# Optimization experiments

Measured on AMD Instinct MI355X. Metric: run time of the kernel, lower is better.

## Reference

```python
import jax, jax.numpy as jnp
import numpy as np

BATCH, NUM, CONS = 16384, 512, 512


def setup_inputs() -> dict:
    key = jax.random.key(0)
    k1, k2, k3, k4 = jax.random.split(key, 4)
    preds = jax.random.uniform(k1, (BATCH, NUM), dtype=jnp.float32)
    # sparse, mutually-exclusive binary body masks (a literal is pos or neg, not both)
    r = jax.random.randint(k2, (CONS, NUM), 0, 12)
    pos_body = (r == 0).astype(jnp.float32)
    neg_body = (r == 1).astype(jnp.float32)
    head_atom = jax.random.randint(k3, (CONS,), 0, NUM).astype(jnp.int32)
    head_sign = jax.random.randint(k4, (CONS,), 0, 2).astype(jnp.bool_)
    return {"preds": preds, "pos_body": pos_body, "neg_body": neg_body,
            "head_atom": head_atom, "head_sign": head_sign}


def reference(preds, pos_body, neg_body, head_atom, head_sign):
    # apply_iterative with goal=None: Gauss-Seidel sweep over constraints.
    # For constraint c: body value per atom j is pos_body[c,j]*(1-p[:,j]) or
    # neg_body[c,j]*p[:,j]; candidate = 1 - max(0, max_j body value);
    # then head literal is raised (positive) or lowered (negative).
    def step(p, xs):
        pos_row, neg_row, atom, sign = xs
        # [batch, num] elementwise; masks are disjoint so per-atom max == concat-max
        vals = jnp.maximum(pos_row[None, :] * (1.0 - p), neg_row[None, :] * p)
        cand = 1.0 - jnp.maximum(jnp.max(vals, axis=1), 0.0)  # zeros column in torch cat
        prev = jnp.take(p, atom, axis=1)  # [batch]
        upd = jnp.where(sign,
                        jnp.maximum(prev, cand),
                        jnp.minimum(prev, 1.0 - cand))
        p = jax.lax.dynamic_update_slice(p, upd[:, None], (0, atom))
        return p, None

    out, _ = jax.lax.scan(step, preds, (pos_body, neg_body, head_atom, head_sign))
    return out
```

## Files before the change

kernel.cpp:

```cpp
#include <hip/hip_runtime.h>

#define BATCH 16384
#define NUM   512
#define CONS  512
#define ROWS  8
#define ZOFF  (NUM*16)
#define OOFF  (NUM*16 + 128)
#define LDSB  (NUM*16 + 256)
#define NPAD  (CONS + 4)
#define RSTR  84

typedef _Float16 h2 __attribute__((ext_vector_type(2)));
static __device__ __forceinline__ h2 u2h(unsigned u){ return __builtin_bit_cast(h2,u); }
static __device__ __forceinline__ unsigned h2u(h2 h){ return __builtin_bit_cast(unsigned,h); }
static __device__ __forceinline__ h2 hmax2(h2 a,h2 b){ return __builtin_elementwise_max(a,b); }
static __device__ __forceinline__ h2 hmin2(h2 a,h2 b){ return __builtin_elementwise_min(a,b); }
template<int C>
static __device__ __forceinline__ h2 dppmax(h2 x) {
  unsigned v = (unsigned)__builtin_amdgcn_mov_dpp((int)h2u(x), C, 0xF, 0xF, true);
  return hmax2(x, u2h(v));
}

__global__ __launch_bounds__(64) void prep_kernel(
    const float* __restrict__ pos, const float* __restrict__ neg,
    const int* __restrict__ head_atom, const int* __restrict__ head_sign,
    unsigned* __restrict__ ents) {
  int c = blockIdx.x, lane = threadIdx.x;
  unsigned* rec = ents + (size_t)c * RSTR;
  if (c >= CONS) {
    for (int t = lane; t < RSTR; t += 64) {
      unsigned v = 0;
      if (t < 32)      { unsigned d = ZOFF + (unsigned)(t & 7) * 16u; v = d | (d << 16); }
      else if (t < 64) { unsigned d = OOFF + (unsigned)(t & 7) * 16u; v = d | (d << 16); }
      else if (t == 64) v = 0x8000u << 16;
      else if (t < 73) v = ZOFF;
      else if (t < 81) v = OOFF;
      rec[t] = v;
    }
    return;
  }
  __shared__ unsigned short LN[96], LP[96];
  __shared__ unsigned short slotN[64], slotP[64];
  __shared__ unsigned char usedN[64], usedP[64];
  __shared__ unsigned short spill[16][8];
  __shared__ int spn[16];
  __shared__ unsigned short exN[8], exP[8];
  __shared__ int exn, exp_;
  slotN[lane] = (unsigned short)(ZOFF + (lane & 7) * 16);
  slotP[lane] = (unsigned short)(OOFF + (lane & 7) * 16);
  usedN[lane] = 0;    usedP[lane] = 0;
  if (lane < 8) { exN[lane] = ZOFF; exP[lane] = OOFF; }
  if (lane < 16) spn[lane] = 0;
  __syncthreads();

  int hp1 = (c >= 1) ? head_atom[c-1] : -1;
  int hp2 = (c >= 2) ? head_atom[c-2] : -1;
  int nN = 0, nP = 0;
  bool fN1=false, fP1=false, fN2=false, fP2=false;
  for (int k = 0; k < NUM/64; ++k) {
    int a = k*64 + lane;
    bool ln = neg[(size_t)c*NUM + a] != 0.f;
    bool lp = pos[(size_t)c*NUM + a] != 0.f;
    bool n1 = ln && (a == hp1), n2 = ln && (a == hp2);
    bool p1 = lp && (a == hp1), p2 = lp && (a == hp2);
    fN1 |= (__ballot(n1) != 0ull); fN2 |= (__ballot(n2) != 0ull);
    fP1 |= (__ballot(p1) != 0ull); fP2 |= (__ballot(p2) != 0ull);
    bool kn = ln && !n1 && !n2;
    bool kp = lp && !p1 && !p2;
    unsigned long long mn = __ballot(kn), mp = __ballot(kp);
    unsigned long long lt = (1ull << lane) - 1ull;
    int rn = nN + (int)__popcll(mn & lt);
    int rp = nP + (int)__popcll(mp & lt);
    if (kn && rn < 96) LN[rn] = (unsigned short)a;
    if (kp && rp < 96) LP[rp] = (unsigned short)a;
    nN += (int)__popcll(mn);
    nP += (int)__popcll(mp);
  }
  __syncthreads();
  if (lane < 16) {
    int r = lane & 7;
    bool isP = lane >= 8;
    const unsigned short* L = isP ? LP : LN;
    int n = isP ? nP : nN; if (n > 96) n = 96;
    unsigned short* slot = isP ? slotP : slotN;
    unsigned char* used = isP ? usedP : usedN;
    int rr = 0;
    for (int t = 0; t < n; ++t) {
      int a = L[t];
      if ((a & 7) == r) {
        if (rr < 8) { int s = rr*8 + r; slot[s] = (unsigned short)(a*16); used[s] = 1; }
        else if (rr < 16) spill[lane][rr-8] = (unsigned short)(a*16);
        ++rr;
      }
    }
    spn[lane] = rr > 8 ? (rr > 16 ? 8 : rr - 8) : 0;
  }
  __syncthreads();
  if (lane < 2) {
    bool isP = lane == 1;
    unsigned short* slot = isP ? slotP : slotN;
    unsigned char* used = isP ? usedP : usedN;
    unsigned short* exb = isP ? exP : exN;
    int base = isP ? 8 : 0;
    int e = 0, scan = 0;
    for (int r = 0; r < 8; ++r) {
      int ns = spn[base + r];
      for (int k = 0; k < ns; ++k) {
        unsigned short v = spill[base + r][k];
        while (scan < 64 && used[scan]) ++scan;
        if (scan < 64) { slot[scan] = v; used[scan] = 1; }
        else if (e < 8) exb[e++] = v;
      }
    }
    if (isP) exp_ = e; else exn = e;
  }
  __syncthreads();

  int hc = head_atom[c];
  unsigned fl = 0;
  if (head_sign[c]) fl |= 1u;
  if (fN1) fl |= 2u;  if (fP1) fl |= 4u;
  if (fN2) fl |= 8u;  if (fP2) fl |= 16u;
  if (hc == hp1) fl |= 32u; else if (hc == hp2) fl |= 64u;
  fl |= ((unsigned)exn << 7) | ((unsigned)exp_ << 11);
  unsigned ho = (unsigned)hc * 16u;
  for (int t = lane; t < RSTR; t += 64) {
    unsigned v;
    if (t < 32) {
      int jp = t >> 4, g = t & 15;
      v = (unsigned)slotN[32*jp + g] | ((unsigned)slotN[32*jp + 16 + g] << 16);
    } else if (t < 64) {
      int tp = t - 32, jp = tp >> 4, g = tp & 15;
      v = (unsigned)slotP[32*jp + g] | ((unsigned)slotP[32*jp + 16 + g] << 16);
    } else if (t == 64) v = ho | (fl << 16);
    else if (t < 73) v = exN[t - 65];
    else if (t < 81) v = exP[t - 73];
    else v = 0;
    rec[t] = v;
  }
}

struct ENT { unsigned w0, w1, w2, w3, mh; };
struct RDv { h2 n0,n1,n2,n3,p0,p1,p2,p3,pv; unsigned mh; };
struct ST  { h2 braw, prevraw; unsigned ho, flu; };

static __device__ __forceinline__ ENT ldent(const unsigned* ents, int c, int g) {
  const unsigned* rec = ents + (size_t)c * RSTR;
  ENT e;
  e.w0 = rec[g]; e.w1 = rec[16+g]; e.w2 = rec[32+g]; e.w3 = rec[48+g];
  e.mh = rec[64];
  return e;
}
static __device__ __forceinline__ void issue_reads(const ENT& E, const char* Pb,
                                                   unsigned pr4, RDv& R) {
  R.n0 = *(const h2*)(Pb + ((E.w0 & 0xFFFFu) + pr4));
  R.n1 = *(const h2*)(Pb + ((E.w0 >> 16)     + pr4));
  R.n2 = *(const h2*)(Pb + ((E.w1 & 0xFFFFu) + pr4));
  R.n3 = *(const h2*)(Pb + ((E.w1 >> 16)     + pr4));
  R.p0 = *(const h2*)(Pb + ((E.w2 & 0xFFFFu) + pr4));
  R.p1 = *(const h2*)(Pb + ((E.w2 >> 16)     + pr4));
  R.p2 = *(const h2*)(Pb + ((E.w3 & 0xFFFFu) + pr4));
  R.p3 = *(const h2*)(Pb + ((E.w3 >> 16)     + pr4));
  R.pv = *(const h2*)(Pb + ((E.mh & 0xFFFFu) + pr4));
  R.mh = E.mh;
}
static __device__ __forceinline__ void combine(const RDv& R, const unsigned* ents,
                                               int c, const char* Pb, unsigned pr4, ST& S) {
  h2 aN = hmax2(hmax2(R.n0, R.n1), hmax2(R.n2, R.n3));
  h2 aP = hmin2(hmin2(R.p0, R.p1), hmin2(R.p2, R.p3));
  unsigned flu = ((unsigned)__builtin_amdgcn_readfirstlane((int)R.mh)) >> 16;
  if (flu & 0x7F80u) {
    const unsigned* rec = ents + (size_t)c * RSTR;
    unsigned xn = (flu >> 7) & 15u, xp = (flu >> 11) & 15u;
    for (unsigned j = 0; j < xn; ++j) aN = hmax2(aN, *(const h2*)(Pb + (rec[65+j] + pr4)));
    for (unsigned j = 0; j < xp; ++j) aP = hmin2(aP, *(const h2*)(Pb + (rec[73+j] + pr4)));
  }
  const h2 one2 = {(_Float16)1.f, (_Float16)1.f};
  h2 bp = hmax2(aN, one2 - aP);
  bp = dppmax<0xB1>(bp);
  bp = dppmax<0x4E>(bp);
  bp = dppmax<0x141>(bp);
  {
    auto sw = __builtin_amdgcn_permlane32_swap((int)h2u(bp), (int)h2u(bp), false, false);
    bp = hmax2(u2h((unsigned)sw[0]), u2h((unsigned)sw[1]));
  }
  S.braw = bp; S.prevraw = R.pv; S.ho = R.mh & 0xFFFFu; S.flu = flu;
}
static __device__ __forceinline__ h2 finalize(const ST& S, h2 up1, h2 up2,
                                              char* Pb, unsigned pr4, int lane) {
  const h2 one2 = {(_Float16)1.f, (_Float16)1.f};
  unsigned fl = S.flu;
  h2 b = S.braw;
  if (fl & 0x1Eu) {
    unsigned mN1 = 0u-((fl>>1)&1u), mP1 = 0u-((fl>>2)&1u);
    unsigned mN2 = 0u-((fl>>3)&1u), mP2 = 0u-((fl>>4)&1u);
    b = hmax2(b, u2h(h2u(up1) & mN1));
    b = hmax2(b, u2h(h2u(one2 - up1) & mP1));
    b = hmax2(b, u2h(h2u(up2) & mN2));
    b = hmax2(b, u2h(h2u(one2 - up2) & mP2));
  }
  h2 prev = S.prevraw;
  if (fl & 0x60u) {
    unsigned mR1 = 0u-((fl>>5)&1u), mR2 = 0u-((fl>>6)&1u), mRn = ~(mR1|mR2);
    prev = u2h((h2u(up1)&mR1) | (h2u(up2)&mR2) | (h2u(S.prevraw)&mRn));
  }
  unsigned ms = 0u-(fl&1u);
  unsigned hi = h2u(hmax2(prev, one2 - b));
  unsigned lo = h2u(hmin2(prev, b));
  h2 upd = u2h((hi&ms) | (lo&~ms));
  if ((lane & 39) == 0 && !(fl & 0x8000u))
    *(h2*)(Pb + S.ho + pr4) = upd;
  return upd;
}

__global__ __launch_bounds__(64, 2) void solve_kernel(
    const float* __restrict__ preds,
    const unsigned* __restrict__ ents,
    float* __restrict__ out) {
  __shared__ char Pb[LDSB];
  const int lane = threadIdx.x;
  const unsigned pr4 = (unsigned)((lane >> 3) & 3) * 4u;
  const int g = (lane & 7) | ((lane >> 5) << 3);
  const int r2s = lane >> 4, cs = lane & 15;
  const size_t row0 = (size_t)blockIdx.x * ROWS;

  if (lane < 32) *(unsigned*)(Pb + ZOFF + lane*4) = 0u;
  else           *(unsigned*)(Pb + OOFF + (lane-32)*4) = 0x3C003C00u;

  for (int i = 0; i < 16; ++i) {
    int a = i*32 + cs*2;
    float2 v0 = *(const float2*)(preds + (row0 + 2*r2s)     * NUM + a);
    float2 v1 = *(const float2*)(preds + (row0 + 2*r2s + 1) * NUM + a);
    h2 w0 = {(_Float16)v0.x, (_Float16)v1.x};
    h2 w1 = {(_Float16)v0.y, (_Float16)v1.y};
    *(h2*)(Pb + a*16 + r2s*4) = w0;
    *(h2*)(Pb + (a+1)*16 + r2s*4) = w1;
  }
  __syncthreads();

  ENT E0 = ldent(ents, 0, g), E1 = ldent(ents, 1, g);
  ENT E2 = ldent(ents, 2, g), E3 = ldent(ents, 3, g);
  RDv RA, RB; ST S0, S1;
  issue_reads(E0, Pb, pr4, RA);
  issue_reads(E1, Pb, pr4, RB);
  combine(RA, ents, 0, Pb, pr4, S0);
  h2 up1 = (h2)0.0f, up2 = (h2)0.0f;

  #pragma unroll 1
  for (int i = 0; i < CONS; i += 2) {
    issue_reads(E2, Pb, pr4, RA);
    { h2 u = finalize(S0, up1, up2, Pb, pr4, lane); up2 = up1; up1 = u; }
    combine(RB, ents, i+1, Pb, pr4, S1);
    E2 = ldent(ents, i+4, g);
    issue_reads(E3, Pb, pr4, RB);
    { h2 u = finalize(S1, up1, up2, Pb, pr4, lane); up2 = up1; up1 = u; }
    combine(RA, ents, i+2, Pb, pr4, S0);
    E3 = ldent(ents, i+5, g);
  }

  __syncthreads();
  for (int i = 0; i < 16; ++i) {
    int a = i*32 + cs*2;
    h2 w0 = *(const h2*)(Pb + a*16 + r2s*4);
    h2 w1 = *(const h2*)(Pb + (a+1)*16 + r2s*4);
    float2 v0 = {(float)w0.x, (float)w1.x};
    float2 v1 = {(float)w0.y, (float)w1.y};
    *(float2*)(out + (row0 + 2*r2s)     * NUM + a) = v0;
    *(float2*)(out + (row0 + 2*r2s + 1) * NUM + a) = v1;
  }
}

extern "C" void kernel_launch(void* const* d_in, const int* in_sizes, int n_in,
                              void* d_out, int out_size, void* d_ws, size_t ws_size,
                              hipStream_t stream) {
  (void)in_sizes; (void)n_in; (void)out_size; (void)ws_size;
  const float* preds     = (const float*)d_in[0];
  const float* pos       = (const float*)d_in[1];
  const float* neg       = (const float*)d_in[2];
  const int*   head_atom = (const int*)d_in[3];
  const int*   head_sign = (const int*)d_in[4];

  unsigned* ents = (unsigned*)d_ws;

  prep_kernel<<<NPAD, 64, 0, stream>>>(pos, neg, head_atom, head_sign, ents);
  solve_kernel<<<BATCH / ROWS, 64, 0, stream>>>(preds, ents, (float*)d_out);
}
```

Measured before the change: 273.7 us.

## Process two constraints per step across wavefront halves with four rows per block

Each workgroup now handles 4 batch rows instead of 8, and the two 32-lane halves of the wavefront evaluate consecutive constraints (a pair) at the same time. The second constraint's dependence on the first is resolved via permlane32 swap and flag masks. The prep kernel now builds paired records with 16 classes of 4 slots, spill handling, and a third-previous-head dependency flag. Occupancy rises to 4 waves per SIMD, and the serial chain per constraint pair gets shorter. The cost is extra select and mask logic, plus more complex and fragile encoding of the cases where the paired constraints depend on each other.

```diff
diff --git a/kernel.cpp b/kernel.cpp
--- a/kernel.cpp
+++ b/kernel.cpp
@@ -3,12 +3,13 @@
 #define BATCH 16384
 #define NUM   512
 #define CONS  512
-#define ROWS  8
-#define ZOFF  (NUM*16)
-#define OOFF  (NUM*16 + 128)
-#define LDSB  (NUM*16 + 256)
-#define NPAD  (CONS + 4)
-#define RSTR  84
+#define ROWS  4
+#define ZOFF  (NUM*8)
+#define OOFF  (NUM*8 + 128)
+#define LDSB  (NUM*8 + 256)
+#define NPAIR 260
+#define NPAD  (2*NPAIR)
+#define RSTR  148
 
 typedef _Float16 h2 __attribute__((ext_vector_type(2)));
 static __device__ __forceinline__ h2 u2h(unsigned u){ return __builtin_bit_cast(h2,u); }
@@ -20,6 +21,13 @@
   unsigned v = (unsigned)__builtin_amdgcn_mov_dpp((int)h2u(x), C, 0xF, 0xF, true);
   return hmax2(x, u2h(v));
 }
+static __device__ __forceinline__ h2 bmask(unsigned mh, int bit) {
+  return u2h((unsigned)(((int)(mh << (31 - bit))) >> 31));
+}
+static __device__ __forceinline__ h2 swap32pair(h2 x, bool hi) {
+  auto r = __builtin_amdgcn_permlane32_swap((int)h2u(x), (int)h2u(x), false, false);
+  return u2h((unsigned)(hi ? r[0] : r[1]));
+}
 
 __global__ __launch_bounds__(64) void prep_kernel(
     const float* __restrict__ pos, const float* __restrict__ neg,
@@ -27,246 +35,272 @@
     unsigned* __restrict__ ents) {
   int c = blockIdx.x, lane = threadIdx.x;
   unsigned* rec = ents + (size_t)c * RSTR;
-  if (c >= CONS) {
-    for (int t = lane; t < RSTR; t += 64) {
-      unsigned v = 0;
-      if (t < 32)      { unsigned d = ZOFF + (unsigned)(t & 7) * 16u; v = d | (d << 16); }
-      else if (t < 64) { unsigned d = OOFF + (unsigned)(t & 7) * 16u; v = d | (d << 16); }
-      else if (t == 64) v = 0x8000u << 16;
-      else if (t < 73) v = ZOFF;
-      else if (t < 81) v = OOFF;
-      rec[t] = v;
-    }
-    return;
-  }
-  __shared__ unsigned short LN[96], LP[96];
   __shared__ unsigned short slotN[64], slotP[64];
-  __shared__ unsigned char usedN[64], usedP[64];
-  __shared__ unsigned short spill[16][8];
-  __shared__ int spn[16];
+  __shared__ unsigned char  usedN[64], usedP[64];
+  __shared__ unsigned short spillN[16][12], spillP[16][12];
+  __shared__ unsigned char  spnN[16], spnP[16];
   __shared__ unsigned short exN[8], exP[8];
   __shared__ int exn, exp_;
-  slotN[lane] = (unsigned short)(ZOFF + (lane & 7) * 16);
-  slotP[lane] = (unsigned short)(OOFF + (lane & 7) * 16);
-  usedN[lane] = 0;    usedP[lane] = 0;
-  if (lane < 8) { exN[lane] = ZOFF; exP[lane] = OOFF; }
-  if (lane < 16) spn[lane] = 0;
+  slotN[lane] = (unsigned short)(ZOFF + (lane & 15) * 8);
+  slotP[lane] = (unsigned short)(OOFF + (lane & 15) * 8);
+  usedN[lane] = 0; usedP[lane] = 0;
+  if (lane < 8)  { exN[lane] = ZOFF; exP[lane] = OOFF; }
+  if (lane < 16) { spnN[lane] = 0;  spnP[lane] = 0; }
+  if (lane == 0) { exn = 0; exp_ = 0; }
   __syncthreads();
 
-  int hp1 = (c >= 1) ? head_atom[c-1] : -1;
-  int hp2 = (c >= 2) ? head_atom[c-2] : -1;
-  int nN = 0, nP = 0;
-  bool fN1=false, fP1=false, fN2=false, fP2=false;
-  for (int k = 0; k < NUM/64; ++k) {
-    int a = k*64 + lane;
-    bool ln = neg[(size_t)c*NUM + a] != 0.f;
-    bool lp = pos[(size_t)c*NUM + a] != 0.f;
-    bool n1 = ln && (a == hp1), n2 = ln && (a == hp2);
-    bool p1 = lp && (a == hp1), p2 = lp && (a == hp2);
-    fN1 |= (__ballot(n1) != 0ull); fN2 |= (__ballot(n2) != 0ull);
-    fP1 |= (__ballot(p1) != 0ull); fP2 |= (__ballot(p2) != 0ull);
-    bool kn = ln && !n1 && !n2;
-    bool kp = lp && !p1 && !p2;
-    unsigned long long mn = __ballot(kn), mp = __ballot(kp);
-    unsigned long long lt = (1ull << lane) - 1ull;
-    int rn = nN + (int)__popcll(mn & lt);
-    int rp = nP + (int)__popcll(mp & lt);
-    if (kn && rn < 96) LN[rn] = (unsigned short)a;
-    if (kp && rp < 96) LP[rp] = (unsigned short)a;
-    nN += (int)__popcll(mn);
-    nP += (int)__popcll(mp);
-  }
-  __syncthreads();
-  if (lane < 16) {
-    int r = lane & 7;
-    bool isP = lane >= 8;
-    const unsigned short* L = isP ? LP : LN;
-    int n = isP ? nP : nN; if (n > 96) n = 96;
-    unsigned short* slot = isP ? slotP : slotN;
-    unsigned char* used = isP ? usedP : usedN;
-    int rr = 0;
-    for (int t = 0; t < n; ++t) {
-      int a = L[t];
-      if ((a & 7) == r) {
-        if (rr < 8) { int s = rr*8 + r; slot[s] = (unsigned short)(a*16); used[s] = 1; }
-        else if (rr < 16) spill[lane][rr-8] = (unsigned short)(a*16);
-        ++rr;
+  unsigned fl = 0, ho = ZOFF;
+  if (c < CONS) {
+    int hp1 = (c >= 1) ? head_atom[c-1] : -1;
+    int hp2 = (c >= 2) ? head_atom[c-2] : -1;
+    int hp3 = ((c & 1) && c >= 3) ? head_atom[c-3] : -1;
+    bool fN1=false,fP1=false,fN2=false,fP2=false,fN3=false,fP3=false;
+    const int myclass = lane & 15;
+    const unsigned long long clsmask = 0x0001000100010001ull << myclass;
+    const unsigned long long lt = (1ull << lane) - 1ull;
+    int cntN = 0, cntP = 0;
+    for (int k = 0; k < NUM/64; ++k) {
+      int a = k*64 + lane;
+      bool ln = neg[(size_t)c*NUM + a] != 0.f;
+      bool lp = pos[(size_t)c*NUM + a] != 0.f;
+      bool i1 = (a == hp1);
+      bool i2 = (a == hp2) && !i1;
+      bool i3 = (a == hp3) && !i1 && (a != hp2);
+      fN1 |= __ballot(ln && i1) != 0ull; fP1 |= __ballot(lp && i1) != 0ull;
+      fN2 |= __ballot(ln && i2) != 0ull; fP2 |= __ballot(lp && i2) != 0ull;
+      fN3 |= __ballot(ln && i3) != 0ull; fP3 |= __ballot(lp && i3) != 0ull;
+      bool kn = ln && !i1 && !i2 && !i3;
+      bool kp = lp && !i1 && !i2 && !i3;
+      unsigned long long mn = __ballot(kn) & clsmask;
+      unsigned long long mp = __ballot(kp) & clsmask;
+      if (kn) {
+        int rr = cntN + (int)__popcll(mn & lt);
+        if (rr < 4) { slotN[rr*16+myclass] = (unsigned short)(a*8); usedN[rr*16+myclass] = 1; }
+        else if (rr < 16) spillN[myclass][rr-4] = (unsigned short)(a*8);
       }
+      if (kp) {
+        int rr = cntP + (int)__popcll(mp & lt);
+        if (rr < 4) { slotP[rr*16+myclass] = (unsigned short)(a*8); usedP[rr*16+myclass] = 1; }
+        else if (rr < 16) spillP[myclass][rr-4] = (unsigned short)(a*8);
+      }
+      cntN += (int)__popcll(mn); cntP += (int)__popcll(mp);
     }
-    spn[lane] = rr > 8 ? (rr > 16 ? 8 : rr - 8) : 0;
-  }
-  __syncthreads();
-  if (lane < 2) {
-    bool isP = lane == 1;
-    unsigned short* slot = isP ? slotP : slotN;
-    unsigned char* used = isP ? usedP : usedN;
-    unsigned short* exb = isP ? exP : exN;
-    int base = isP ? 8 : 0;
-    int e = 0, scan = 0;
-    for (int r = 0; r < 8; ++r) {
-      int ns = spn[base + r];
-      for (int k = 0; k < ns; ++k) {
-        unsigned short v = spill[base + r][k];
-        while (scan < 64 && used[scan]) ++scan;
-        if (scan < 64) { slot[scan] = v; used[scan] = 1; }
-        else if (e < 8) exb[e++] = v;
+    if (lane < 16) {
+      int sn = cntN - 4; if (sn < 0) sn = 0; if (sn > 12) sn = 12;
+      int sp = cntP - 4; if (sp < 0) sp = 0; if (sp > 12) sp = 12;
+      spnN[lane] = (unsigned char)sn; spnP[lane] = (unsigned char)sp;
+    }
+    __syncthreads();
+    if (lane < 2) {
+      bool isP = lane == 1;
+      unsigned short* slot = isP ? slotP : slotN;
+      unsigned char*  used = isP ? usedP : usedN;
+      unsigned char*  spn  = isP ? spnP  : spnN;
+      unsigned short* exb  = isP ? exP   : exN;
+      int e = 0, scan = 0;
+      for (int r = 0; r < 16; ++r) {
+        int ns = spn[r];
+        for (int k = 0; k < ns; ++k) {
+          unsigned short v = isP ? spillP[r][k] : spillN[r][k];
+          while (scan < 64 && used[scan]) ++scan;
+          if (scan < 64) { slot[scan] = v; used[scan] = 1; }
+          else if (e < 7) exb[e++] = v;
+        }
       }
+      if (isP) exp_ = e; else exn = e;
     }
-    if (isP) exp_ = e; else exn = e;
-  }
-  __syncthreads();
-
-  int hc = head_atom[c];
-  unsigned fl = 0;
-  if (head_sign[c]) fl |= 1u;
-  if (fN1) fl |= 2u;  if (fP1) fl |= 4u;
-  if (fN2) fl |= 8u;  if (fP2) fl |= 16u;
-  if (hc == hp1) fl |= 32u; else if (hc == hp2) fl |= 64u;
-  fl |= ((unsigned)exn << 7) | ((unsigned)exp_ << 11);
-  unsigned ho = (unsigned)hc * 16u;
+    __syncthreads();
+    int hc = head_atom[c];
+    fl = (head_sign[c] ? 1u : 0u)
+       | (fN1?2u:0u) | (fP1?4u:0u) | (fN2?8u:0u) | (fP2?16u:0u);
+    unsigned rcode = (hc==hp1) ? 1u : (hc==hp2) ? 2u : (hc==hp3) ? 3u : 0u;
+    fl |= rcode << 5;
+    fl |= ((unsigned)exn) << 7;
+    fl |= ((unsigned)exp_) << 10;
+    if (fN3) fl |= 1u << 13;
+    if (fP3) fl |= 1u << 14;
+    if (!(c & 1) && (c + 1) < CONS && head_atom[c+1] == hc) fl |= 0x8000u;
+    ho = (unsigned)hc * 8u;
+  } else {
+    fl = 0x8000u;
+  }
+
   for (int t = lane; t < RSTR; t += 64) {
     unsigned v;
-    if (t < 32) {
-      int jp = t >> 4, g = t & 15;
-      v = (unsigned)slotN[32*jp + g] | ((unsigned)slotN[32*jp + 16 + g] << 16);
-    } else if (t < 64) {
-      int tp = t - 32, jp = tp >> 4, g = tp & 15;
-      v = (unsigned)slotP[32*jp + g] | ((unsigned)slotP[32*jp + 16 + g] << 16);
-    } else if (t == 64) v = ho | (fl << 16);
-    else if (t < 73) v = exN[t - 65];
-    else if (t < 81) v = exP[t - 73];
+    if (t < 130) {
+      int copy = (t >= 65) ? 1 : 0;
+      int u = t - copy*65;
+      unsigned pr = (unsigned)copy * 4u;
+      if (u == 64) v = (ho + pr) | (fl << 16);
+      else {
+        int gg = u & 15, blk = u >> 4;
+        const unsigned short* arr = (blk >= 2) ? slotP : slotN;
+        int base = (blk & 1) * 32;
+        v = ((unsigned)arr[base+gg] + pr) | ((((unsigned)arr[base+16+gg]) + pr) << 16);
+      }
+    } else if (t < 138) v = exN[t-130];
+    else if (t < 146) v = exP[t-138];
     else v = 0;
     rec[t] = v;
   }
 }
 
-struct ENT { unsigned w0, w1, w2, w3, mh; };
-struct RDv { h2 n0,n1,n2,n3,p0,p1,p2,p3,pv; unsigned mh; };
-struct ST  { h2 braw, prevraw; unsigned ho, flu; };
-
-static __device__ __forceinline__ ENT ldent(const unsigned* ents, int c, int g) {
-  const unsigned* rec = ents + (size_t)c * RSTR;
-  ENT e;
-  e.w0 = rec[g]; e.w1 = rec[16+g]; e.w2 = rec[32+g]; e.w3 = rec[48+g];
-  e.mh = rec[64];
+struct PENT { unsigned r0, r1, r2, r3, rm; };
+struct RDv  { h2 n0,n1,n2,n3,p0,p1,p2,p3,pv; unsigned mh; };
+struct ST   { h2 bp, pv; unsigned mh, su; };
+
+static __device__ __forceinline__ PENT pld(const unsigned* ents, int p, int lo, int lm) {
+  const unsigned* bp = ents + (size_t)(2*p) * RSTR;
+  PENT e;
+  e.r0 = bp[lo]; e.r1 = bp[lo+16]; e.r2 = bp[lo+32]; e.r3 = bp[lo+48]; e.rm = bp[lm];
   return e;
 }
-static __device__ __forceinline__ void issue_reads(const ENT& E, const char* Pb,
-                                                   unsigned pr4, RDv& R) {
-  R.n0 = *(const h2*)(Pb + ((E.w0 & 0xFFFFu) + pr4));
-  R.n1 = *(const h2*)(Pb + ((E.w0 >> 16)     + pr4));
-  R.n2 = *(const h2*)(Pb + ((E.w1 & 0xFFFFu) + pr4));
-  R.n3 = *(const h2*)(Pb + ((E.w1 >> 16)     + pr4));
-  R.p0 = *(const h2*)(Pb + ((E.w2 & 0xFFFFu) + pr4));
-  R.p1 = *(const h2*)(Pb + ((E.w2 >> 16)     + pr4));
-  R.p2 = *(const h2*)(Pb + ((E.w3 & 0xFFFFu) + pr4));
-  R.p3 = *(const h2*)(Pb + ((E.w3 >> 16)     + pr4));
-  R.pv = *(const h2*)(Pb + ((E.mh & 0xFFFFu) + pr4));
-  R.mh = E.mh;
-}
-static __device__ __forceinline__ void combine(const RDv& R, const unsigned* ents,
-                                               int c, const char* Pb, unsigned pr4, ST& S) {
-  h2 aN = hmax2(hmax2(R.n0, R.n1), hmax2(R.n2, R.n3));
-  h2 aP = hmin2(hmin2(R.p0, R.p1), hmin2(R.p2, R.p3));
-  unsigned flu = ((unsigned)__builtin_amdgcn_readfirstlane((int)R.mh)) >> 16;
-  if (flu & 0x7F80u) {
-    const unsigned* rec = ents + (size_t)c * RSTR;
-    unsigned xn = (flu >> 7) & 15u, xp = (flu >> 11) & 15u;
-    for (unsigned j = 0; j < xn; ++j) aN = hmax2(aN, *(const h2*)(Pb + (rec[65+j] + pr4)));
-    for (unsigned j = 0; j < xp; ++j) aP = hmin2(aP, *(const h2*)(Pb + (rec[73+j] + pr4)));
+static __device__ __forceinline__ void issue(const PENT& E, const char* Pb, RDv& R) {
+  R.n0 = *(const h2*)(Pb + (E.r0 & 0xFFFFu));
+  R.n1 = *(const h2*)(Pb + (E.r0 >> 16));
+  R.n2 = *(const h2*)(Pb + (E.r1 & 0xFFFFu));
+  R.n3 = *(const h2*)(Pb + (E.r1 >> 16));
+  R.p0 = *(const h2*)(Pb + (E.r2 & 0xFFFFu));
+  R.p1 = *(const h2*)(Pb + (E.r2 >> 16));
+  R.p2 = *(const h2*)(Pb + (E.r3 & 0xFFFFu));
+  R.p3 = *(const h2*)(Pb + (E.r3 >> 16));
+  R.pv = *(const h2*)(Pb + (E.rm & 0xFFFFu));
+  R.mh = E.rm;
+}
+static __device__ __forceinline__ void comb(const RDv& R, const unsigned* __restrict__ ents,
+    int p, int half, unsigned pr4b, const char* Pb, ST& S) {
+  h2 aN = hmax2(hmax2(R.n0,R.n1), hmax2(R.n2,R.n3));
+  h2 aP = hmin2(hmin2(R.p0,R.p1), hmin2(R.p2,R.p3));
+  unsigned s0 = (unsigned)__builtin_amdgcn_readfirstlane((int)R.mh);
+  unsigned s1 = (unsigned)__builtin_amdgcn_readlane((int)R.mh, 32);
+  unsigned su = s0 | s1;
+  if (su & 0x1F800000u) {
+    unsigned xa = (s0>>23)&7u, xb = (s1>>23)&7u; unsigned xn = xa>xb?xa:xb;
+    unsigned ya = (s0>>26)&7u, yb = (s1>>26)&7u; unsigned xp = ya>yb?ya:yb;
+    const unsigned* rp_ = ents + (size_t)(2*p + half) * RSTR;
+    for (unsigned j = 0; j < xn; ++j) aN = hmax2(aN, *(const h2*)(Pb + (rp_[130+j] + pr4b)));
+    for (unsigned j = 0; j < xp; ++j) aP = hmin2(aP, *(const h2*)(Pb + (rp_[138+j] + pr4b)));
   }
   const h2 one2 = {(_Float16)1.f, (_Float16)1.f};
-  h2 bp = hmax2(aN, one2 - aP);
-  bp = dppmax<0xB1>(bp);
-  bp = dppmax<0x4E>(bp);
-  bp = dppmax<0x141>(bp);
-  {
-    auto sw = __builtin_amdgcn_permlane32_swap((int)h2u(bp), (int)h2u(bp), false, false);
-    bp = hmax2(u2h((unsigned)sw[0]), u2h((unsigned)sw[1]));
-  }
-  S.braw = bp; S.prevraw = R.pv; S.ho = R.mh & 0xFFFFu; S.flu = flu;
-}
-static __device__ __forceinline__ h2 finalize(const ST& S, h2 up1, h2 up2,
-                                              char* Pb, unsigned pr4, int lane) {
+  h2 b = hmax2(aN, one2 - aP);
+  b = dppmax<0xB1>(b);
+  b = dppmax<0x4E>(b);
+  b = dppmax<0x141>(b);
+  b = dppmax<0x140>(b);
+  S.bp = b; S.pv = R.pv; S.mh = R.mh; S.su = su;
+}
+static __device__ __forceinline__ void fin(const ST& S, h2& u1, h2& u2,
+    char* Pb, bool hi32, bool wl) {
   const h2 one2 = {(_Float16)1.f, (_Float16)1.f};
-  unsigned fl = S.flu;
-  h2 b = S.braw;
-  if (fl & 0x1Eu) {
-    unsigned mN1 = 0u-((fl>>1)&1u), mP1 = 0u-((fl>>2)&1u);
-    unsigned mN2 = 0u-((fl>>3)&1u), mP2 = 0u-((fl>>4)&1u);
-    b = hmax2(b, u2h(h2u(up1) & mN1));
-    b = hmax2(b, u2h(h2u(one2 - up1) & mP1));
-    b = hmax2(b, u2h(h2u(up2) & mN2));
-    b = hmax2(b, u2h(h2u(one2 - up2) & mP2));
-  }
-  h2 prev = S.prevraw;
-  if (fl & 0x60u) {
-    unsigned mR1 = 0u-((fl>>5)&1u), mR2 = 0u-((fl>>6)&1u), mRn = ~(mR1|mR2);
-    prev = u2h((h2u(up1)&mR1) | (h2u(up2)&mR2) | (h2u(S.prevraw)&mRn));
-  }
-  unsigned ms = 0u-(fl&1u);
-  unsigned hi = h2u(hmax2(prev, one2 - b));
-  unsigned lo = h2u(hmin2(prev, b));
-  h2 upd = u2h((hi&ms) | (lo&~ms));
-  if ((lane & 39) == 0 && !(fl & 0x8000u))
-    *(h2*)(Pb + S.ho + pr4) = upd;
-  return upd;
-}
-
-__global__ __launch_bounds__(64, 2) void solve_kernel(
+  unsigned mh = S.mh, su = S.su;
+  bool pbr = (su & 0x601E0000u) != 0;
+  bool rbr = (su & 0x00600000u) != 0;
+  h2 b1 = S.bp;
+  if (pbr) {
+    b1 = hmax2(b1, u2h(h2u(u1)        & h2u(bmask(mh,17))));
+    b1 = hmax2(b1, u2h(h2u(one2 - u1) & h2u(bmask(mh,18))));
+    b1 = hmax2(b1, u2h(h2u(u2)        & h2u(bmask(mh,19))));
+    b1 = hmax2(b1, u2h(h2u(one2 - u2) & h2u(bmask(mh,20))));
+  }
+  h2 prev1 = S.pv;
+  if (rbr) {
+    unsigned code = (mh >> 21) & 3u;
+    prev1 = (code == 1u) ? u1 : prev1;
+    prev1 = (code == 2u) ? u2 : prev1;
+  }
+  h2 ms = bmask(mh,16);
+  h2 t1; { h2 hi = hmax2(prev1, one2 - b1); h2 lo = hmin2(prev1, b1);
+           t1 = u2h((h2u(hi)&h2u(ms)) | (h2u(lo)&~h2u(ms))); }
+  h2 upd = t1;
+  if (pbr | rbr) {
+    h2 x1 = swap32pair(t1, hi32);
+    h2 b2 = S.bp;
+    b2 = hmax2(b2, u2h(h2u(x1)        & h2u(bmask(mh,17))));
+    b2 = hmax2(b2, u2h(h2u(one2 - x1) & h2u(bmask(mh,18))));
+    b2 = hmax2(b2, u2h(h2u(u1)        & h2u(bmask(mh,19))));
+    b2 = hmax2(b2, u2h(h2u(one2 - u1) & h2u(bmask(mh,20))));
+    b2 = hmax2(b2, u2h(h2u(u2)        & h2u(bmask(mh,29))));
+    b2 = hmax2(b2, u2h(h2u(one2 - u2) & h2u(bmask(mh,30))));
+    h2 prev2 = S.pv;
+    if (rbr) {
+      unsigned code = (mh >> 21) & 3u;
+      prev2 = (code == 1u) ? x1 : prev2;
+      prev2 = (code == 2u) ? u1 : prev2;
+      prev2 = (code == 3u) ? u2 : prev2;
+    }
+    h2 t2; { h2 hi = hmax2(prev2, one2 - b2); h2 lo = hmin2(prev2, b2);
+             t2 = u2h((h2u(hi)&h2u(ms)) | (h2u(lo)&~h2u(ms))); }
+    upd = hi32 ? t2 : t1;
+  }
+  if (wl && !(mh & 0x80000000u))
+    *(h2*)(Pb + (mh & 0xFFFFu)) = upd;
+  h2 sw = swap32pair(upd, hi32);
+  u2 = hi32 ? sw  : upd;
+  u1 = hi32 ? upd : sw;
+}
+
+__global__ __launch_bounds__(64, 4) void solve_kernel(
     const float* __restrict__ preds,
     const unsigned* __restrict__ ents,
     float* __restrict__ out) {
   __shared__ char Pb[LDSB];
   const int lane = threadIdx.x;
-  const unsigned pr4 = (unsigned)((lane >> 3) & 3) * 4u;
-  const int g = (lane & 7) | ((lane >> 5) << 3);
-  const int r2s = lane >> 4, cs = lane & 15;
+  const int g    = lane & 15;
+  const int r2i  = (lane >> 4) & 1;
+  const int half = lane >> 5;
+  const bool hi32 = half != 0;
+  const bool wl   = (lane & 15) == 0;
+  const unsigned pr4b = (unsigned)r2i * 4u;
+  const int lo = half*RSTR + r2i*65 + g;
+  const int lm = half*RSTR + r2i*65 + 64;
   const size_t row0 = (size_t)blockIdx.x * ROWS;
+  const int rp = lane >> 5, col = lane & 31;
 
   if (lane < 32) *(unsigned*)(Pb + ZOFF + lane*4) = 0u;
   else           *(unsigned*)(Pb + OOFF + (lane-32)*4) = 0x3C003C00u;
 
-  for (int i = 0; i < 16; ++i) {
-    int a = i*32 + cs*2;
-    float2 v0 = *(const float2*)(preds + (row0 + 2*r2s)     * NUM + a);
-    float2 v1 = *(const float2*)(preds + (row0 + 2*r2s + 1) * NUM + a);
+  for (int i = 0; i < 8; ++i) {
+    int a = i*64 + col*2;
+    float2 v0 = *(const float2*)(preds + (row0 + 2*rp)     * NUM + a);
+    float2 v1 = *(const float2*)(preds + (row0 + 2*rp + 1) * NUM + a);
     h2 w0 = {(_Float16)v0.x, (_Float16)v1.x};
     h2 w1 = {(_Float16)v0.y, (_Float16)v1.y};
-    *(h2*)(Pb + a*16 + r2s*4) = w0;
-    *(h2*)(Pb + (a+1)*16 + r2s*4) = w1;
+    *(h2*)(Pb + a*8 + rp*4) = w0;
+    *(h2*)(Pb + (a+1)*8 + rp*4) = w1;
   }
   __syncthreads();
 
-  ENT E0 = ldent(ents, 0, g), E1 = ldent(ents, 1, g);
-  ENT E2 = ldent(ents, 2, g), E3 = ldent(ents, 3, g);
-  RDv RA, RB; ST S0, S1;
-  issue_reads(E0, Pb, pr4, RA);
-  issue_reads(E1, Pb, pr4, RB);
-  combine(RA, ents, 0, Pb, pr4, S0);
-  h2 up1 = (h2)0.0f, up2 = (h2)0.0f;
+  PENT A = pld(ents, 0, lo, lm), B = pld(ents, 1, lo, lm);
+  PENT C = pld(ents, 2, lo, lm), D = pld(ents, 3, lo, lm);
+  RDv Ra, Rb; ST S;
+  issue(A, Pb, Ra);
+  h2 u1 = (h2)0.0f, u2 = (h2)0.0f;
 
   #pragma unroll 1
-  for (int i = 0; i < CONS; i += 2) {
-    issue_reads(E2, Pb, pr4, RA);
-    { h2 u = finalize(S0, up1, up2, Pb, pr4, lane); up2 = up1; up1 = u; }
-    combine(RB, ents, i+1, Pb, pr4, S1);
-    E2 = ldent(ents, i+4, g);
-    issue_reads(E3, Pb, pr4, RB);
-    { h2 u = finalize(S1, up1, up2, Pb, pr4, lane); up2 = up1; up1 = u; }
-    combine(RA, ents, i+2, Pb, pr4, S0);
-    E3 = ldent(ents, i+5, g);
+  for (int q = 0; q < 256; q += 4) {
+    issue(B, Pb, Rb);
+    A = pld(ents, q+4, lo, lm);
+    comb(Ra, ents, q,   half, pr4b, Pb, S); fin(S, u1, u2, Pb, hi32, wl);
+    issue(C, Pb, Ra);
+    B = pld(ents, q+5, lo, lm);
+    comb(Rb, ents, q+1, half, pr4b, Pb, S); fin(S, u1, u2, Pb, hi32, wl);
+    issue(D, Pb, Rb);
+    C = pld(ents, q+6, lo, lm);
+    comb(Ra, ents, q+2, half, pr4b, Pb, S); fin(S, u1, u2, Pb, hi32, wl);
+    issue(A, Pb, Ra);
+    D = pld(ents, q+7, lo, lm);
+    comb(Rb, ents, q+3, half, pr4b, Pb, S); fin(S, u1, u2, Pb, hi32, wl);
   }
 
   __syncthreads();
-  for (int i = 0; i < 16; ++i) {
-    int a = i*32 + cs*2;
-    h2 w0 = *(const h2*)(Pb + a*16 + r2s*4);
-    h2 w1 = *(const h2*)(Pb + (a+1)*16 + r2s*4);
+  for (int i = 0; i < 8; ++i) {
+    int a = i*64 + col*2;
+    h2 w0 = *(const h2*)(Pb + a*8 + rp*4);
+    h2 w1 = *(const h2*)(Pb + (a+1)*8 + rp*4);
     float2 v0 = {(float)w0.x, (float)w1.x};
     float2 v1 = {(float)w0.y, (float)w1.y};
-    *(float2*)(out + (row0 + 2*r2s)     * NUM + a) = v0;
-    *(float2*)(out + (row0 + 2*r2s + 1) * NUM + a) = v1;
+    *(float2*)(out + (row0 + 2*rp)     * NUM + a) = v0;
+    *(float2*)(out + (row0 + 2*rp + 1) * NUM + a) = v1;
   }
 }
 
```

New measurement: 302.9 us. 1.11x slower.

## Deepen constraint software pipeline to three-ahead and streamline prep slot assignment

Applied to the files above, without the earlier changes.

The main sweep now keeps three constraints' LDS reads in flight, up from one, using four rotating read buffers and a 4-way unrolled loop. The aim is to hide LDS read latency behind the serial combine/finalize chain. Each constraint is read three steps ahead, so correctness relies on the up1/up2 patch mechanism (flags for the previous two heads) still covering every stale read. The prep kernel also assigns slots directly from ballot counts per residue class, dropping the list-building pass and a sync, and NPAD grows to cover the extra lookahead padding records.

```diff
diff --git a/kernel.cpp b/kernel.cpp
--- a/kernel.cpp
+++ b/kernel.cpp
@@ -7,7 +7,7 @@
 #define ZOFF  (NUM*16)
 #define OOFF  (NUM*16 + 128)
 #define LDSB  (NUM*16 + 256)
-#define NPAD  (CONS + 4)
+#define NPAD  520
 #define RSTR  84
 
 typedef _Float16 h2 __attribute__((ext_vector_type(2)));
@@ -27,111 +27,95 @@
     unsigned* __restrict__ ents) {
   int c = blockIdx.x, lane = threadIdx.x;
   unsigned* rec = ents + (size_t)c * RSTR;
-  if (c >= CONS) {
-    for (int t = lane; t < RSTR; t += 64) {
-      unsigned v = 0;
-      if (t < 32)      { unsigned d = ZOFF + (unsigned)(t & 7) * 16u; v = d | (d << 16); }
-      else if (t < 64) { unsigned d = OOFF + (unsigned)(t & 7) * 16u; v = d | (d << 16); }
-      else if (t == 64) v = 0x8000u << 16;
-      else if (t < 73) v = ZOFF;
-      else if (t < 81) v = OOFF;
-      rec[t] = v;
-    }
-    return;
-  }
-  __shared__ unsigned short LN[96], LP[96];
   __shared__ unsigned short slotN[64], slotP[64];
-  __shared__ unsigned char usedN[64], usedP[64];
-  __shared__ unsigned short spill[16][8];
-  __shared__ int spn[16];
+  __shared__ unsigned char  usedN[64], usedP[64];
+  __shared__ unsigned short spillN[8][12], spillP[8][12];
+  __shared__ unsigned char  spnN[8], spnP[8];
   __shared__ unsigned short exN[8], exP[8];
   __shared__ int exn, exp_;
   slotN[lane] = (unsigned short)(ZOFF + (lane & 7) * 16);
   slotP[lane] = (unsigned short)(OOFF + (lane & 7) * 16);
-  usedN[lane] = 0;    usedP[lane] = 0;
-  if (lane < 8) { exN[lane] = ZOFF; exP[lane] = OOFF; }
-  if (lane < 16) spn[lane] = 0;
+  usedN[lane] = 0; usedP[lane] = 0;
+  if (lane < 8) { exN[lane] = ZOFF; exP[lane] = OOFF; spnN[lane] = 0; spnP[lane] = 0; }
+  if (lane == 0) { exn = 0; exp_ = 0; }
   __syncthreads();
 
-  int hp1 = (c >= 1) ? head_atom[c-1] : -1;
-  int hp2 = (c >= 2) ? head_atom[c-2] : -1;
-  int nN = 0, nP = 0;
-  bool fN1=false, fP1=false, fN2=false, fP2=false;
-  for (int k = 0; k < NUM/64; ++k) {
-    int a = k*64 + lane;
-    bool ln = neg[(size_t)c*NUM + a] != 0.f;
-    bool lp = pos[(size_t)c*NUM + a] != 0.f;
-    bool n1 = ln && (a == hp1), n2 = ln && (a == hp2);
-    bool p1 = lp && (a == hp1), p2 = lp && (a == hp2);
-    fN1 |= (__ballot(n1) != 0ull); fN2 |= (__ballot(n2) != 0ull);
-    fP1 |= (__ballot(p1) != 0ull); fP2 |= (__ballot(p2) != 0ull);
-    bool kn = ln && !n1 && !n2;
-    bool kp = lp && !p1 && !p2;
-    unsigned long long mn = __ballot(kn), mp = __ballot(kp);
-    unsigned long long lt = (1ull << lane) - 1ull;
-    int rn = nN + (int)__popcll(mn & lt);
-    int rp = nP + (int)__popcll(mp & lt);
-    if (kn && rn < 96) LN[rn] = (unsigned short)a;
-    if (kp && rp < 96) LP[rp] = (unsigned short)a;
-    nN += (int)__popcll(mn);
-    nP += (int)__popcll(mp);
-  }
-  __syncthreads();
-  if (lane < 16) {
-    int r = lane & 7;
-    bool isP = lane >= 8;
-    const unsigned short* L = isP ? LP : LN;
-    int n = isP ? nP : nN; if (n > 96) n = 96;
-    unsigned short* slot = isP ? slotP : slotN;
-    unsigned char* used = isP ? usedP : usedN;
-    int rr = 0;
-    for (int t = 0; t < n; ++t) {
-      int a = L[t];
-      if ((a & 7) == r) {
-        if (rr < 8) { int s = rr*8 + r; slot[s] = (unsigned short)(a*16); used[s] = 1; }
-        else if (rr < 16) spill[lane][rr-8] = (unsigned short)(a*16);
-        ++rr;
+  unsigned fl = 0, ho = ZOFF;
+  if (c < CONS) {
+    int hp1 = (c >= 1) ? head_atom[c-1] : -1;
+    int hp2 = (c >= 2) ? head_atom[c-2] : -1;
+    bool fN1=false, fP1=false, fN2=false, fP2=false;
+    const int res = lane & 7;
+    const unsigned long long clsmask = 0x0101010101010101ull << res;
+    const unsigned long long lt = (1ull << lane) - 1ull;
+    int cntN = 0, cntP = 0;
+    for (int k = 0; k < NUM/64; ++k) {
+      int a = k*64 + lane;
+      bool ln = neg[(size_t)c*NUM + a] != 0.f;
+      bool lp = pos[(size_t)c*NUM + a] != 0.f;
+      bool i1 = (a == hp1);
+      bool i2 = (a == hp2) && !i1;
+      fN1 |= __ballot(ln && i1) != 0ull; fP1 |= __ballot(lp && i1) != 0ull;
+      fN2 |= __ballot(ln && i2) != 0ull; fP2 |= __ballot(lp && i2) != 0ull;
+      bool kn = ln && !i1 && !i2;
+      bool kp = lp && !i1 && !i2;
+      unsigned long long mn = __ballot(kn) & clsmask;
+      unsigned long long mp = __ballot(kp) & clsmask;
+      if (kn) {
+        int rr = cntN + (int)__popcll(mn & lt);
+        if (rr < 8) { slotN[rr*8+res] = (unsigned short)(a*16); usedN[rr*8+res] = 1; }
+        else if (rr < 20) spillN[res][rr-8] = (unsigned short)(a*16);
       }
+      if (kp) {
+        int rr = cntP + (int)__popcll(mp & lt);
+        if (rr < 8) { slotP[rr*8+res] = (unsigned short)(a*16); usedP[rr*8+res] = 1; }
+        else if (rr < 20) spillP[res][rr-8] = (unsigned short)(a*16);
+      }
+      cntN += (int)__popcll(mn); cntP += (int)__popcll(mp);
     }
-    spn[lane] = rr > 8 ? (rr > 16 ? 8 : rr - 8) : 0;
-  }
-  __syncthreads();
-  if (lane < 2) {
-    bool isP = lane == 1;
-    unsigned short* slot = isP ? slotP : slotN;
-    unsigned char* used = isP ? usedP : usedN;
-    unsigned short* exb = isP ? exP : exN;
-    int base = isP ? 8 : 0;
-    int e = 0, scan = 0;
-    for (int r = 0; r < 8; ++r) {
-      int ns = spn[base + r];
-      for (int k = 0; k < ns; ++k) {
-        unsigned short v = spill[base + r][k];
-        while (scan < 64 && used[scan]) ++scan;
-        if (scan < 64) { slot[scan] = v; used[scan] = 1; }
-        else if (e < 8) exb[e++] = v;
+    if (lane < 8) {
+      int sn = cntN - 8; if (sn < 0) sn = 0; if (sn > 12) sn = 12;
+      int sp = cntP - 8; if (sp < 0) sp = 0; if (sp > 12) sp = 12;
+      spnN[lane] = (unsigned char)sn; spnP[lane] = (unsigned char)sp;
+    }
+    __syncthreads();
+    if (lane < 2) {
+      bool isP = lane == 1;
+      unsigned short* slot = isP ? slotP : slotN;
+      unsigned char*  used = isP ? usedP : usedN;
+      unsigned char*  spn  = isP ? spnP  : spnN;
+      unsigned short* exb  = isP ? exP   : exN;
+      int e = 0, scan = 0;
+      for (int r = 0; r < 8; ++r) {
+        int ns = spn[r];
+        for (int k = 0; k < ns; ++k) {
+          unsigned short v = isP ? spillP[r][k] : spillN[r][k];
+          while (scan < 64 && used[scan]) ++scan;
+          if (scan < 64) { slot[scan] = v; used[scan] = 1; }
+          else if (e < 8) exb[e++] = v;
+        }
       }
+      if (isP) exp_ = e; else exn = e;
     }
-    if (isP) exp_ = e; else exn = e;
-  }
-  __syncthreads();
-
-  int hc = head_atom[c];
-  unsigned fl = 0;
-  if (head_sign[c]) fl |= 1u;
-  if (fN1) fl |= 2u;  if (fP1) fl |= 4u;
-  if (fN2) fl |= 8u;  if (fP2) fl |= 16u;
-  if (hc == hp1) fl |= 32u; else if (hc == hp2) fl |= 64u;
-  fl |= ((unsigned)exn << 7) | ((unsigned)exp_ << 11);
-  unsigned ho = (unsigned)hc * 16u;
+    __syncthreads();
+    int hc = head_atom[c];
+    fl = (head_sign[c] ? 1u : 0u)
+       | (fN1?2u:0u) | (fP1?4u:0u) | (fN2?8u:0u) | (fP2?16u:0u);
+    if (hc == hp1) fl |= 32u; else if (hc == hp2) fl |= 64u;
+    fl |= ((unsigned)exn << 7) | ((unsigned)exp_ << 11);
+    ho = (unsigned)hc * 16u;
+  } else {
+    fl = 0x8000u;
+  }
+
   for (int t = lane; t < RSTR; t += 64) {
     unsigned v;
     if (t < 32) {
-      int jp = t >> 4, g = t & 15;
-      v = (unsigned)slotN[32*jp + g] | ((unsigned)slotN[32*jp + 16 + g] << 16);
+      int jp = t >> 4, gg = t & 15;
+      v = (unsigned)slotN[32*jp + gg] | ((unsigned)slotN[32*jp + 16 + gg] << 16);
     } else if (t < 64) {
-      int tp = t - 32, jp = tp >> 4, g = tp & 15;
-      v = (unsigned)slotP[32*jp + g] | ((unsigned)slotP[32*jp + 16 + g] << 16);
+      int tp = t - 32, jp = tp >> 4, gg = tp & 15;
+      v = (unsigned)slotP[32*jp + gg] | ((unsigned)slotP[32*jp + 16 + gg] << 16);
     } else if (t == 64) v = ho | (fl << 16);
     else if (t < 73) v = exN[t - 65];
     else if (t < 81) v = exP[t - 73];
@@ -238,24 +222,38 @@
   }
   __syncthreads();
 
-  ENT E0 = ldent(ents, 0, g), E1 = ldent(ents, 1, g);
-  ENT E2 = ldent(ents, 2, g), E3 = ldent(ents, 3, g);
-  RDv RA, RB; ST S0, S1;
-  issue_reads(E0, Pb, pr4, RA);
-  issue_reads(E1, Pb, pr4, RB);
-  combine(RA, ents, 0, Pb, pr4, S0);
+  ENT Ea = ldent(ents, 3, g), Eb = ldent(ents, 4, g);
+  ENT Ec = ldent(ents, 5, g), Ed = ldent(ents, 6, g);
+  RDv Ra, Rb, Rc, Rd; ST S;
+  {
+    ENT t0 = ldent(ents, 0, g), t1 = ldent(ents, 1, g), t2 = ldent(ents, 2, g);
+    issue_reads(t0, Pb, pr4, Ra);
+    issue_reads(t1, Pb, pr4, Rb);
+    issue_reads(t2, Pb, pr4, Rc);
+  }
   h2 up1 = (h2)0.0f, up2 = (h2)0.0f;
 
   #pragma unroll 1
-  for (int i = 0; i < CONS; i += 2) {
-    issue_reads(E2, Pb, pr4, RA);
-    { h2 u = finalize(S0, up1, up2, Pb, pr4, lane); up2 = up1; up1 = u; }
-    combine(RB, ents, i+1, Pb, pr4, S1);
-    E2 = ldent(ents, i+4, g);
-    issue_reads(E3, Pb, pr4, RB);
-    { h2 u = finalize(S1, up1, up2, Pb, pr4, lane); up2 = up1; up1 = u; }
-    combine(RA, ents, i+2, Pb, pr4, S0);
-    E3 = ldent(ents, i+5, g);
+  for (int q = 0; q < CONS; q += 4) {
+    combine(Ra, ents, q, Pb, pr4, S);
+    { h2 u = finalize(S, up1, up2, Pb, pr4, lane); up2 = up1; up1 = u; }
+    issue_reads(Ea, Pb, pr4, Rd);
+    Ea = ldent(ents, q+7, g);
+
+    combine(Rb, ents, q+1, Pb, pr4, S);
+    { h2 u = finalize(S, up1, up2, Pb, pr4, lane); up2 = up1; up1 = u; }
+    issue_reads(Eb, Pb, pr4, Ra);
+    Eb = ldent(ents, q+8, g);
+
+    combine(Rc, ents, q+2, Pb, pr4, S);
+    { h2 u = finalize(S, up1, up2, Pb, pr4, lane); up2 = up1; up1 = u; }
+    issue_reads(Ec, Pb, pr4, Rb);
+    Ec = ldent(ents, q+9, g);
+
+    combine(Rd, ents, q+3, Pb, pr4, S);
+    { h2 u = finalize(S, up1, up2, Pb, pr4, lane); up2 = up1; up1 = u; }
+    issue_reads(Ed, Pb, pr4, Rc);
+    Ed = ldent(ents, q+10, g);
   }
 
   __syncthreads();
```

After: 285.0 us. +4.2%, slower.
